# Kernel tuning notes

Hardware: AMD Instinct MI355X
Metric: run time of the kernel (lower is better)

## Reference

```python
import jax, jax.numpy as jnp
import numpy as np

B, S, D, H, F = 4, 2048, 1024, 16, 4096
HD = D // H
EPS = 1e-5


def _xavier(key, shape, fan_in, fan_out):
    a = float(np.sqrt(6.0 / (fan_in + fan_out)))
    return jax.random.uniform(key, shape, jnp.float32, -a, a)


def setup_inputs() -> dict:
    key = jax.random.key(0)
    ks = jax.random.split(key, 8)
    x = jax.random.normal(ks[0], (B, S, D), jnp.float32)
    # torch xavier_uniform on (1,H,D,HD) uses fan_in=D, fan_out=HD
    Wq = _xavier(ks[1], (H, D, HD), D, HD)
    Wk = _xavier(ks[2], (H, D, HD), D, HD)
    Wv = _xavier(ks[3], (H, D, HD), D, HD)
    Wo = _xavier(ks[4], (D, D), D, D)
    w_in = _xavier(ks[5], (D, F), D, F)
    b_in = jnp.zeros((F,), jnp.float32)
    w_out = _xavier(ks[6], (F, D), F, D)
    b_out = jnp.zeros((D,), jnp.float32)
    g1 = jnp.ones((D,), jnp.float32)
    be1 = jnp.zeros((D,), jnp.float32)
    g2 = jnp.ones((D,), jnp.float32)
    be2 = jnp.zeros((D,), jnp.float32)
    return {"x": x, "Wq": Wq, "Wk": Wk, "Wv": Wv, "Wo": Wo,
            "g1": g1, "be1": be1, "w_in": w_in, "b_in": b_in,
            "w_out": w_out, "b_out": b_out, "g2": g2, "be2": be2}


def _layernorm(x, g, b):
    mu = jnp.mean(x, axis=-1, keepdims=True)
    var = jnp.mean(jnp.square(x - mu), axis=-1, keepdims=True)
    return (x - mu) * jax.lax.rsqrt(var + EPS) * g + b


def reference(x, Wq, Wk, Wv, Wo, g1, be1, w_in, b_in, w_out, b_out, g2, be2):
    b, s, d = x.shape
    h, _, hd = Wq.shape
    q = jnp.einsum('bsd,hde->bhse', x, Wq)
    k = jnp.einsum('bsd,hde->bhse', x, Wk)
    v = jnp.einsum('bsd,hde->bhse', x, Wv)
    scores = jnp.einsum('bhse,bhte->bhst', q, k) / jnp.sqrt(jnp.float32(hd))
    causal = jnp.triu(jnp.ones((s, s), bool), k=1)  # [S,S]
    scores = jnp.where(causal, -jnp.inf, scores)
    p = jax.nn.softmax(scores, axis=-1)
    attn = jnp.einsum('bhst,bhte->bhse', p, v)
    # torch .view on contiguous (B,H,S,hd) -> (B,S,H*hd): plain reshape (no transpose)
    attn = attn.reshape(b, s, h * hd)
    attn = attn @ Wo
    x = _layernorm(x + attn, g1, be1)
    ffn = jax.nn.relu(x @ w_in + b_in) @ w_out + b_out
    x = _layernorm(x + ffn, g2, be2)
    return x
```

## Files before the change

### kernel.cpp

```cpp
#include <hip/hip_runtime.h>
#include <hip/hip_bf16.h>

typedef __hip_bfloat16 bf16;

#define BB 4
#define SS 2048
#define DD 1024
#define HH 16
#define FF 4096
#define HD 64
#define LN_EPS 1e-5f
#define QSCALE 0.1803368801111204f

typedef __attribute__((ext_vector_type(8))) __bf16 bf16x8;
typedef __attribute__((ext_vector_type(8))) unsigned short u16x8;
typedef __attribute__((ext_vector_type(4))) float f32x4;

__device__ __forceinline__ float cvt(float v) { return v; }
__device__ __forceinline__ float cvt(bf16 v) { return __bfloat162float(v); }
__device__ __forceinline__ void stf(float* p, float v) { *p = v; }
__device__ __forceinline__ void stf(bf16* p, float v) { *p = __float2bfloat16(v); }

__device__ __forceinline__ unsigned short f2bf_rne(float x) {
    unsigned int u = __float_as_uint(x);
    unsigned int r = (u + 0x7fffu + ((u >> 16) & 1u)) >> 16;
    return (unsigned short)r;
}

__device__ __forceinline__ void async_cp16(const void* g, void* l) {
    __builtin_amdgcn_global_load_lds(
        (const __attribute__((address_space(1))) unsigned int*)g,
        (__attribute__((address_space(3))) unsigned int*)l, 16, 0, 0);
}

__device__ __forceinline__ u16x8 ld_f32_chunk(const float* p) {
    const float4* q = (const float4*)p;
    const float4 a = q[0], b = q[1];
    u16x8 r;
    r[0] = f2bf_rne(a.x); r[1] = f2bf_rne(a.y); r[2] = f2bf_rne(a.z); r[3] = f2bf_rne(a.w);
    r[4] = f2bf_rne(b.x); r[5] = f2bf_rne(b.y); r[6] = f2bf_rne(b.z); r[7] = f2bf_rne(b.w);
    return r;
}

template <typename TA, typename TC, int EPI>
__launch_bounds__(256)
__global__ void mfma_gemm(const TA* __restrict__ A, const bf16* __restrict__ Bt,
                          TC* __restrict__ C, const float* __restrict__ bias,
                          const bf16* __restrict__ resb,
                          bf16* __restrict__ C2, bf16* __restrict__ C3,
                          int M, int N, int K, float oscale) {
    constexpr bool AF = (sizeof(TA) == 4);
    __shared__ unsigned short As[128 * 64];
    __shared__ unsigned short Bs[128 * 64];

    const int tid = threadIdx.x;
    const int lane = tid & 63;
    const int w = tid >> 6;
    const int wm = w >> 1, wn = w & 1;

    const int nwg = gridDim.x * gridDim.y;
    const int id = blockIdx.y * gridDim.x + blockIdx.x;
    const int cpx = nwg >> 3;
    const int swz = (id & 7) * cpx + (id >> 3);
    const int bx = swz % gridDim.x, by = swz / gridDim.x;
    const int m0 = by * 128, n0 = bx * 128;

    int ff[4], fr[4], fc[4], fg[4];
#pragma unroll
    for (int i = 0; i < 4; ++i) {
        ff[i] = tid + i * 256;
        fr[i] = ff[i] >> 3;
        fc[i] = ff[i] & 7;
        fg[i] = fc[i] ^ (fr[i] & 7);
    }

    f32x4 acc[4][4];
#pragma unroll
    for (int i = 0; i < 4; ++i)
#pragma unroll
        for (int j = 0; j < 4; ++j) acc[i][j] = (f32x4){0.f, 0.f, 0.f, 0.f};

    u16x8 sa[4];
    if (AF) {
#pragma unroll
        for (int i = 0; i < 4; ++i)
            sa[i] = ld_f32_chunk((const float*)A + (size_t)(m0 + fr[i]) * K + fg[i] * 8);
    }

    for (int k0 = 0; k0 < K; k0 += 64) {
        if (k0 > 0) __syncthreads();
        if (AF) {
#pragma unroll
            for (int i = 0; i < 4; ++i)
                *(u16x8*)&As[ff[i] * 8] = sa[i];
        } else {
#pragma unroll
            for (int i = 0; i < 4; ++i)
                async_cp16((const unsigned short*)A + (size_t)(m0 + fr[i]) * K + k0 + fg[i] * 8,
                           &As[ff[i] * 8]);
        }
#pragma unroll
        for (int i = 0; i < 4; ++i)
            async_cp16((const unsigned short*)Bt + (size_t)(n0 + fr[i]) * K + k0 + fg[i] * 8,
                       &Bs[ff[i] * 8]);
        __syncthreads();

        if (AF && k0 + 64 < K) {
            const int kn = k0 + 64;
#pragma unroll
            for (int i = 0; i < 4; ++i)
                sa[i] = ld_f32_chunk((const float*)A + (size_t)(m0 + fr[i]) * K + kn + fg[i] * 8);
        }

#pragma unroll
        for (int ks = 0; ks < 2; ++ks) {
            bf16x8 af[4], bfr[4];
#pragma unroll
            for (int i = 0; i < 4; ++i) {
                const int row = wm * 64 + i * 16 + (lane & 15);
                const int col = wn * 64 + i * 16 + (lane & 15);
                const int g = ks * 4 + (lane >> 4);
                af[i]  = *(const bf16x8*)&As[row * 64 + (g ^ (row & 7)) * 8];
                bfr[i] = *(const bf16x8*)&Bs[col * 64 + (g ^ (col & 7)) * 8];
            }
#pragma unroll
            for (int i = 0; i < 4; ++i)
#pragma unroll
                for (int j = 0; j < 4; ++j)
                    acc[i][j] = __builtin_amdgcn_mfma_f32_16x16x32_bf16(
                        af[i], bfr[j], acc[i][j], 0, 0, 0);
        }
    }

#pragma unroll
    for (int i = 0; i < 4; ++i) {
        const int mrow0 = m0 + wm * 64 + i * 16 + (lane >> 4) * 4;
#pragma unroll
        for (int j = 0; j < 4; ++j) {
            const int n = n0 + wn * 64 + j * 16 + (lane & 15);
            if (EPI == 5) {
                const int reg = n >> 10;
                const int nn = n & 1023;
                if (reg == 0) {
#pragma unroll
                    for (int r = 0; r < 4; ++r)
                        stf((bf16*)C + (size_t)(mrow0 + r) * 1024 + nn, acc[i][j][r] * oscale);
                } else if (reg == 1) {
#pragma unroll
                    for (int r = 0; r < 4; ++r)
                        stf(C2 + (size_t)(mrow0 + r) * 1024 + nn, acc[i][j][r]);
                } else {
                    const int bb = mrow0 >> 11, s = mrow0 & 2047;
                    ushort4 pk;
                    pk.x = f2bf_rne(acc[i][j][0]);
                    pk.y = f2bf_rne(acc[i][j][1]);
                    pk.z = f2bf_rne(acc[i][j][2]);
                    pk.w = f2bf_rne(acc[i][j][3]);
                    *(ushort4*)((unsigned short*)C3 + ((size_t)bb * 1024 + nn) * SS + s) = pk;
                }
            } else {
#pragma unroll
                for (int r = 0; r < 4; ++r) {
                    const size_t idx = (size_t)(mrow0 + r) * N + n;
                    float v = acc[i][j][r];
                    if (EPI == 0) v *= oscale;
                    if (EPI == 2) { v += bias[n]; v = fmaxf(v, 0.0f); }
                    if (EPI == 6) v += bias[n] + cvt(resb[idx]);
                    if (EPI == 7) v += cvt(resb[idx]);
                    stf(&C[idx], v);
                }
            }
        }
    }
}

__launch_bounds__(256)
__global__ void prep_kernel(const float* __restrict__ x,
                            const float* __restrict__ Wq, const float* __restrict__ Wk,
                            const float* __restrict__ Wv, const float* __restrict__ Wo,
                            const float* __restrict__ w_in, const float* __restrict__ w_out,
                            bf16* __restrict__ xb, bf16* __restrict__ WqkvT,
                            bf16* __restrict__ WoT, bf16* __restrict__ w_inT,
                            bf16* __restrict__ w_outT) {
    const int id = blockIdx.x;
    if (id < 8192) {
        const int i = id * 256 + threadIdx.x;
        const float4 v = ((const float4*)x)[i];
        ushort4 p;
        p.x = f2bf_rne(v.x); p.y = f2bf_rne(v.y); p.z = f2bf_rne(v.z); p.w = f2bf_rne(v.w);
        ((ushort4*)xb)[i] = p;
        return;
    }
    __shared__ float t[32][33];
    const int rem = id - 8192;
    const float* in;
    bf16* out;
    int R, C, bx, by;
    size_t in_o = 0, out_o = 0;
    if (rem < 3072) {
        const int z = rem >> 6, r2 = rem & 63;
        const int wi = z >> 4, head = z & 15;
        in = (wi == 0) ? Wq : (wi == 1) ? Wk : Wv;
        in_o = (size_t)head * DD * HD;
        out = WqkvT;
        out_o = (size_t)wi * DD * DD + (size_t)head * HD * DD;
        R = DD; C = HD;
        bx = (r2 & 1) * 32; by = (r2 >> 1) * 32;
    } else if (rem < 3072 + 1024) {
        const int r2 = rem - 3072;
        in = Wo; out = WoT; R = DD; C = DD;
        bx = (r2 & 31) * 32; by = (r2 >> 5) * 32;
    } else if (rem < 3072 + 1024 + 4096) {
        const int r2 = rem - 3072 - 1024;
        in = w_in; out = w_inT; R = DD; C = FF;
        bx = (r2 & 127) * 32; by = (r2 >> 7) * 32;
    } else {
        const int r2 = rem - 3072 - 1024 - 4096;
        in = w_out; out = w_outT; R = FF; C = DD;
        bx = (r2 & 31) * 32; by = (r2 >> 5) * 32;
    }
    const int tx = threadIdx.x & 31, ty = threadIdx.x >> 5;
#pragma unroll
    for (int i = 0; i < 32; i += 8)
        t[ty + i][tx] = in[in_o + (size_t)(by + ty + i) * C + bx + tx];
    __syncthreads();
#pragma unroll
    for (int i = 0; i < 32; i += 8)
        out[out_o + (size_t)(bx + ty + i) * R + by + tx] = __float2bfloat16(t[tx][ty + i]);
}

__launch_bounds__(256, 4)
__global__ void attn_mfma(const bf16* __restrict__ Q, const bf16* __restrict__ K,
                          const bf16* __restrict__ VT, bf16* __restrict__ O) {
    __shared__ unsigned short Ks[64 * 64];
    __shared__ unsigned short Vs[64 * 64];
    __shared__ unsigned short Ps[64 * 72];

    const int tid = threadIdx.x;
    const int lane = tid & 63;
    const int w = tid >> 6;
    const int ln = lane & 15;
    const int qd = lane >> 4;
    const int bh = blockIdx.x;
    const int b = bh >> 4;
    const int h = bh & 15;
    const int qi = 31 - blockIdx.y;
    const int q0 = qi * 64;

    bf16x8 aq[2];
    {
        const unsigned short* qp =
            (const unsigned short*)Q + ((size_t)b * SS + q0 + w * 16 + ln) * DD + h * HD;
        aq[0] = *(const bf16x8*)(qp + qd * 8);
        aq[1] = *(const bf16x8*)(qp + 32 + qd * 8);
    }

    int sf[2], sr[2], sg[2];
#pragma unroll
    for (int i = 0; i < 2; ++i) {
        sf[i] = tid + i * 256;
        sr[i] = sf[i] >> 3;
        sg[i] = (sf[i] & 7) ^ (sr[i] & 7);
    }
    const unsigned short* kbase = (const unsigned short*)K + (size_t)b * SS * DD + h * HD;
    const unsigned short* vbase = (const unsigned short*)VT + (size_t)(b * DD + h * HD) * SS;

    f32x4 oacc[4];
#pragma unroll
    for (int e = 0; e < 4; ++e) oacc[e] = (f32x4){0.f, 0.f, 0.f, 0.f};
    float l_r[4] = {0.f, 0.f, 0.f, 0.f};

    for (int kt = 0; kt <= qi; ++kt) {
        const int t0 = kt * 64;
        __syncthreads();
#pragma unroll
        for (int i = 0; i < 2; ++i) {
            async_cp16(kbase + (size_t)(t0 + sr[i]) * DD + sg[i] * 8, &Ks[sf[i] * 8]);
            async_cp16(vbase + (size_t)sr[i] * SS + t0 + sg[i] * 8, &Vs[sf[i] * 8]);
        }
        __syncthreads();

        f32x4 sfr[4];
#pragma unroll
        for (int ct = 0; ct < 4; ++ct) {
            const int row = ct * 16 + ln;
            const bf16x8 b0 = *(const bf16x8*)&Ks[row * 64 + ((qd) ^ (row & 7)) * 8];
            const bf16x8 b1 = *(const bf16x8*)&Ks[row * 64 + ((4 + qd) ^ (row & 7)) * 8];
            f32x4 t = __builtin_amdgcn_mfma_f32_16x16x32_bf16(
                aq[0], b0, (f32x4){0.f, 0.f, 0.f, 0.f}, 0, 0, 0);
            sfr[ct] = __builtin_amdgcn_mfma_f32_16x16x32_bf16(aq[1], b1, t, 0, 0, 0);
        }

        if (kt == qi) {
#pragma unroll
            for (int ct = 0; ct < 4; ++ct) {
                const int tg = t0 + ct * 16 + ln;
#pragma unroll
                for (int r = 0; r < 4; ++r) {
                    const int qg = q0 + w * 16 + qd * 4 + r;
                    if (tg > qg) sfr[ct][r] = -1e30f;
                }
            }
        }

#pragma unroll
        for (int ct = 0; ct < 4; ++ct)
#pragma unroll
            for (int r = 0; r < 4; ++r)
                sfr[ct][r] = __builtin_amdgcn_exp2f(sfr[ct][r]);
#pragma unroll
        for (int r = 0; r < 4; ++r)
            l_r[r] += (sfr[0][r] + sfr[1][r]) + (sfr[2][r] + sfr[3][r]);

#pragma unroll
        for (int ct = 0; ct < 4; ++ct)
#pragma unroll
            for (int r = 0; r < 4; ++r)
                Ps[(w * 16 + qd * 4 + r) * 72 + ct * 16 + ln] = f2bf_rne(sfr[ct][r]);
        const bf16x8 ap0 = *(const bf16x8*)&Ps[(w * 16 + ln) * 72 + qd * 8];
        const bf16x8 ap1 = *(const bf16x8*)&Ps[(w * 16 + ln) * 72 + 32 + qd * 8];

#pragma unroll
        for (int et = 0; et < 4; ++et) {
            const int row = et * 16 + ln;
            const bf16x8 v0 = *(const bf16x8*)&Vs[row * 64 + ((qd) ^ (row & 7)) * 8];
            const bf16x8 v1 = *(const bf16x8*)&Vs[row * 64 + ((4 + qd) ^ (row & 7)) * 8];
            oacc[et] = __builtin_amdgcn_mfma_f32_16x16x32_bf16(ap0, v0, oacc[et], 0, 0, 0);
            oacc[et] = __builtin_amdgcn_mfma_f32_16x16x32_bf16(ap1, v1, oacc[et], 0, 0, 0);
        }
    }

#pragma unroll
    for (int st = 1; st <= 8; st <<= 1)
#pragma unroll
        for (int r = 0; r < 4; ++r)
            l_r[r] += __shfl_xor(l_r[r], st);
    float linv[4];
#pragma unroll
    for (int r = 0; r < 4; ++r) linv[r] = 1.0f / l_r[r];
    unsigned short* ob = (unsigned short*)O + (size_t)bh * SS * HD;
#pragma unroll
    for (int et = 0; et < 4; ++et)
#pragma unroll
        for (int r = 0; r < 4; ++r) {
            const int qg = q0 + w * 16 + qd * 4 + r;
            ob[(size_t)qg * HD + et * 16 + ln] = f2bf_rne(oacc[et][r] * linv[r]);
        }
}

template <typename TIN, typename TOUT>
__launch_bounds__(256)
__global__ void ln_kernel(const TIN* __restrict__ X, TOUT* __restrict__ Y,
                          const float* __restrict__ g, const float* __restrict__ be) {
    const int row = blockIdx.x;
    const int tid = threadIdx.x;
    const int lane = tid & 63, w = tid >> 6;
    __shared__ float red[8];
    __shared__ float mv[2];

    float4 v;
    if (sizeof(TIN) == 4) {
        v = ((const float4*)((const float*)X + (size_t)row * DD))[tid];
    } else {
        const ushort4 u = ((const ushort4*)((const unsigned short*)X + (size_t)row * DD))[tid];
        v.x = __uint_as_float((unsigned)u.x << 16);
        v.y = __uint_as_float((unsigned)u.y << 16);
        v.z = __uint_as_float((unsigned)u.z << 16);
        v.w = __uint_as_float((unsigned)u.w << 16);
    }
    float s = (v.x + v.y) + (v.z + v.w);
    float q = (v.x * v.x + v.y * v.y) + (v.z * v.z + v.w * v.w);
#pragma unroll
    for (int st = 1; st < 64; st <<= 1) {
        s += __shfl_xor(s, st);
        q += __shfl_xor(q, st);
    }
    if (lane == 0) { red[w] = s; red[4 + w] = q; }
    __syncthreads();
    if (tid == 0) {
        const float ts = (red[0] + red[1]) + (red[2] + red[3]);
        const float tq = (red[4] + red[5]) + (red[6] + red[7]);
        const float mu = ts * (1.0f / DD);
        mv[0] = mu;
        mv[1] = rsqrtf(tq * (1.0f / DD) - mu * mu + LN_EPS);
    }
    __syncthreads();
    const float mu = mv[0], rs = mv[1];
    const float4 gg = ((const float4*)g)[tid];
    const float4 bb = ((const float4*)be)[tid];
    float o[4];
    o[0] = (v.x - mu) * rs * gg.x + bb.x;
    o[1] = (v.y - mu) * rs * gg.y + bb.y;
    o[2] = (v.z - mu) * rs * gg.z + bb.z;
    o[3] = (v.w - mu) * rs * gg.w + bb.w;
    if (sizeof(TOUT) == 4) {
        float4 of = {o[0], o[1], o[2], o[3]};
        ((float4*)((float*)Y + (size_t)row * DD))[tid] = of;
    } else {
        ushort4 p;
        p.x = f2bf_rne(o[0]); p.y = f2bf_rne(o[1]);
        p.z = f2bf_rne(o[2]); p.w = f2bf_rne(o[3]);
        ((ushort4*)((unsigned short*)Y + (size_t)row * DD))[tid] = p;
    }
}

extern "C" void kernel_launch(void* const* d_in, const int* in_sizes, int n_in,
                              void* d_out, int out_size, void* d_ws, size_t ws_size,
                              hipStream_t stream) {
    const float* x = (const float*)d_in[0];
    const float* Wq = (const float*)d_in[1];
    const float* Wk = (const float*)d_in[2];
    const float* Wv = (const float*)d_in[3];
    const float* Wo = (const float*)d_in[4];
    const float* g1 = (const float*)d_in[5];
    const float* be1 = (const float*)d_in[6];
    const float* w_in = (const float*)d_in[7];
    const float* b_in = (const float*)d_in[8];
    const float* w_out = (const float*)d_in[9];
    const float* b_out = (const float*)d_in[10];
    const float* g2 = (const float*)d_in[11];
    const float* be2 = (const float*)d_in[12];
    float* out = (float*)d_out;

    char* wsb = (char*)d_ws;
    const size_t MiB = 1u << 20;
    bf16* Qb = (bf16*)(wsb);
    bf16* Kb = (bf16*)(wsb + 16 * MiB);
    bf16* VT = (bf16*)(wsb + 32 * MiB);
    bf16* At = (bf16*)(wsb + 48 * MiB);
    bf16* xb = (bf16*)(wsb + 64 * MiB);
    bf16* X1b = (bf16*)(wsb + 80 * MiB);
    bf16* Hd = (bf16*)(wsb);
    bf16* X2b = (bf16*)(wsb + 64 * MiB);
    bf16* WqkvT = (bf16*)(wsb + 96 * MiB);
    bf16* WoT = (bf16*)(wsb + 102 * MiB);
    bf16* w_inT = (bf16*)(wsb + 104 * MiB);
    bf16* w_outT = (bf16*)(wsb + 112 * MiB);
    (void)ws_size;

    const int M = BB * SS;
    dim3 blk(256);

    prep_kernel<<<dim3(8192 + 3072 + 1024 + 4096 + 4096), blk, 0, stream>>>(
        x, Wq, Wk, Wv, Wo, w_in, w_out, xb, WqkvT, WoT, w_inT, w_outT);

    mfma_gemm<bf16, bf16, 5><<<dim3(3 * DD / 128, M / 128), blk, 0, stream>>>(
        xb, WqkvT, Qb, nullptr, nullptr, Kb, VT, M, 3 * DD, DD, QSCALE);

    attn_mfma<<<dim3(BB * HH, SS / 64), blk, 0, stream>>>(Qb, Kb, VT, At);

    mfma_gemm<bf16, bf16, 7><<<dim3(DD / 128, M / 128), blk, 0, stream>>>(
        At, WoT, X1b, nullptr, xb, nullptr, nullptr, M, DD, DD, 1.0f);
    ln_kernel<bf16, bf16><<<dim3(M), blk, 0, stream>>>(X1b, X1b, g1, be1);

    mfma_gemm<bf16, bf16, 2><<<dim3(FF / 128, M / 128), blk, 0, stream>>>(
        X1b, w_inT, Hd, b_in, nullptr, nullptr, nullptr, M, FF, DD, 1.0f);

    mfma_gemm<bf16, bf16, 6><<<dim3(DD / 128, M / 128), blk, 0, stream>>>(
        Hd, w_outT, X2b, b_out, X1b, nullptr, nullptr, M, DD, FF, 1.0f);

    ln_kernel<bf16, float><<<dim3(M), blk, 0, stream>>>(X2b, out, g2, be2);
}
```

Baseline: 462.4 us.

## Replace GEMM with 256-row double-buffered 8-wave kernel with async prefetch

Swaps the 128x128 single-buffered GEMM for a 256xBN tile kernel with 512 threads, double-buffered LDS, and direct global-to-LDS prefetch issued two k-tiles ahead, gated by explicit vmcnt waits and raw barriers. MFMA issue is split into four phases with raised wave priority, and the FFN up-projection uses a 256x256 tile. The aim is to hide global load latency behind MFMA work and raise arithmetic intensity per block. In exchange, LDS use and register pressure go up, and the larger tiles mean fewer workgroups for the smaller N=1024 GEMMs.

```diff
diff --git a/kernel.cpp b/kernel.cpp
--- a/kernel.cpp
+++ b/kernel.cpp
@@ -33,111 +33,146 @@
         (__attribute__((address_space(3))) unsigned int*)l, 16, 0, 0);
 }
 
-__device__ __forceinline__ u16x8 ld_f32_chunk(const float* p) {
-    const float4* q = (const float4*)p;
-    const float4 a = q[0], b = q[1];
-    u16x8 r;
-    r[0] = f2bf_rne(a.x); r[1] = f2bf_rne(a.y); r[2] = f2bf_rne(a.z); r[3] = f2bf_rne(a.w);
-    r[4] = f2bf_rne(b.x); r[5] = f2bf_rne(b.y); r[6] = f2bf_rne(b.z); r[7] = f2bf_rne(b.w);
-    return r;
-}
-
-template <typename TA, typename TC, int EPI>
-__launch_bounds__(256)
-__global__ void mfma_gemm(const TA* __restrict__ A, const bf16* __restrict__ Bt,
-                          TC* __restrict__ C, const float* __restrict__ bias,
-                          const bf16* __restrict__ resb,
-                          bf16* __restrict__ C2, bf16* __restrict__ C3,
-                          int M, int N, int K, float oscale) {
-    constexpr bool AF = (sizeof(TA) == 4);
-    __shared__ unsigned short As[128 * 64];
-    __shared__ unsigned short Bs[128 * 64];
+template <int N>
+__device__ __forceinline__ void s_wait_vmcnt() {
+    asm volatile("s_waitcnt vmcnt(%0)" ::"n"(N) : "memory");
+    __builtin_amdgcn_sched_barrier(0);
+}
+
+__device__ __forceinline__ void sync_raw() {
+    asm volatile("" ::: "memory");
+    __builtin_amdgcn_s_barrier();
+    asm volatile("" ::: "memory");
+    __builtin_amdgcn_sched_barrier(0);
+}
+
+template <int BN, int WM, int WN, int EPI>
+__launch_bounds__(512, 2)
+__global__ void gemm256(const bf16* __restrict__ Abf, const bf16* __restrict__ Bt,
+                        bf16* __restrict__ C, const float* __restrict__ bias,
+                        const bf16* __restrict__ resb,
+                        bf16* __restrict__ C2, bf16* __restrict__ C3,
+                        int M, int N, int K, float oscale) {
+    static_assert(WM * WN == 8, "8 waves");
+    constexpr int BM = 256;
+    constexpr int PWM = BM / WM;
+    constexpr int PWN = BN / WN;
+    constexpr int MI = PWM / 16;
+    constexpr int NJ = PWN / 16;
+    constexpr int ACH = BM * 8 / 512;
+    constexpr int BCH = BN * 8 / 512;
+    constexpr int LPT = ACH + BCH;
+
+    __shared__ unsigned short As[2][BM * 64];
+    __shared__ unsigned short Bs[2][BN * 64];
 
     const int tid = threadIdx.x;
     const int lane = tid & 63;
     const int w = tid >> 6;
-    const int wm = w >> 1, wn = w & 1;
+    const int wm = w / WN, wn = w % WN;
+    const int ln = lane & 15;
+    const int qd = lane >> 4;
 
     const int nwg = gridDim.x * gridDim.y;
     const int id = blockIdx.y * gridDim.x + blockIdx.x;
     const int cpx = nwg >> 3;
     const int swz = (id & 7) * cpx + (id >> 3);
     const int bx = swz % gridDim.x, by = swz / gridDim.x;
-    const int m0 = by * 128, n0 = bx * 128;
-
-    int ff[4], fr[4], fc[4], fg[4];
-#pragma unroll
-    for (int i = 0; i < 4; ++i) {
-        ff[i] = tid + i * 256;
-        fr[i] = ff[i] >> 3;
-        fc[i] = ff[i] & 7;
-        fg[i] = fc[i] ^ (fr[i] & 7);
-    }
-
-    f32x4 acc[4][4];
-#pragma unroll
-    for (int i = 0; i < 4; ++i)
-#pragma unroll
-        for (int j = 0; j < 4; ++j) acc[i][j] = (f32x4){0.f, 0.f, 0.f, 0.f};
-
-    u16x8 sa[4];
-    if (AF) {
-#pragma unroll
-        for (int i = 0; i < 4; ++i)
-            sa[i] = ld_f32_chunk((const float*)A + (size_t)(m0 + fr[i]) * K + fg[i] * 8);
-    }
-
-    for (int k0 = 0; k0 < K; k0 += 64) {
-        if (k0 > 0) __syncthreads();
-        if (AF) {
-#pragma unroll
-            for (int i = 0; i < 4; ++i)
-                *(u16x8*)&As[ff[i] * 8] = sa[i];
-        } else {
-#pragma unroll
-            for (int i = 0; i < 4; ++i)
-                async_cp16((const unsigned short*)A + (size_t)(m0 + fr[i]) * K + k0 + fg[i] * 8,
-                           &As[ff[i] * 8]);
-        }
-#pragma unroll
-        for (int i = 0; i < 4; ++i)
-            async_cp16((const unsigned short*)Bt + (size_t)(n0 + fr[i]) * K + k0 + fg[i] * 8,
-                       &Bs[ff[i] * 8]);
-        __syncthreads();
-
-        if (AF && k0 + 64 < K) {
-            const int kn = k0 + 64;
-#pragma unroll
-            for (int i = 0; i < 4; ++i)
-                sa[i] = ld_f32_chunk((const float*)A + (size_t)(m0 + fr[i]) * K + kn + fg[i] * 8);
-        }
-
-#pragma unroll
-        for (int ks = 0; ks < 2; ++ks) {
-            bf16x8 af[4], bfr[4];
-#pragma unroll
-            for (int i = 0; i < 4; ++i) {
-                const int row = wm * 64 + i * 16 + (lane & 15);
-                const int col = wn * 64 + i * 16 + (lane & 15);
-                const int g = ks * 4 + (lane >> 4);
-                af[i]  = *(const bf16x8*)&As[row * 64 + (g ^ (row & 7)) * 8];
-                bfr[i] = *(const bf16x8*)&Bs[col * 64 + (g ^ (col & 7)) * 8];
+    const int m0 = by * BM, n0 = bx * BN;
+
+    const unsigned short* Ag = (const unsigned short*)Abf;
+    const unsigned short* Bg = (const unsigned short*)Bt;
+
+    const unsigned short* agp[ACH];
+    const unsigned short* bgp[BCH];
+    int affo[ACH], bffo[BCH];
+#pragma unroll
+    for (int i = 0; i < ACH; ++i) {
+        const int ff = tid + i * 512, fr = ff >> 3, fg = (ff & 7) ^ (fr & 7);
+        agp[i] = Ag + (size_t)(m0 + fr) * K + fg * 8;
+        affo[i] = ff * 8;
+    }
+#pragma unroll
+    for (int i = 0; i < BCH; ++i) {
+        const int ff = tid + i * 512, fr = ff >> 3, fg = (ff & 7) ^ (fr & 7);
+        bgp[i] = Bg + (size_t)(n0 + fr) * K + fg * 8;
+        bffo[i] = ff * 8;
+    }
+
+    auto stage = [&](int kt, int buf) {
+        const int ko = kt * 64;
+#pragma unroll
+        for (int i = 0; i < ACH; ++i)
+            async_cp16(agp[i] + ko, &As[buf][affo[i]]);
+#pragma unroll
+        for (int i = 0; i < BCH; ++i)
+            async_cp16(bgp[i] + ko, &Bs[buf][bffo[i]]);
+    };
+
+    f32x4 acc[MI][NJ];
+#pragma unroll
+    for (int i = 0; i < MI; ++i)
+#pragma unroll
+        for (int j = 0; j < NJ; ++j) acc[i][j] = (f32x4){0.f, 0.f, 0.f, 0.f};
+
+    const int nt = K >> 6;
+    stage(0, 0);
+    stage(1, 1);
+
+    for (int t = 0; t < nt; ++t) {
+        if (t < nt - 1) s_wait_vmcnt<LPT>();
+        else            s_wait_vmcnt<0>();
+        sync_raw();
+
+        const int buf = t & 1;
+#pragma unroll
+        for (int ph = 0; ph < 4; ++ph) {
+            const int mh = ph >> 1, nh = ph & 1;
+            bf16x8 af[MI / 2][2], bq[NJ / 2][2];
+#pragma unroll
+            for (int i = 0; i < MI / 2; ++i) {
+                const int row = wm * PWM + (mh * (MI / 2) + i) * 16 + ln;
+#pragma unroll
+                for (int ks = 0; ks < 2; ++ks) {
+                    const int g = ks * 4 + qd;
+                    af[i][ks] = *(const bf16x8*)&As[buf][row * 64 + (g ^ (row & 7)) * 8];
+                }
             }
 #pragma unroll
-            for (int i = 0; i < 4; ++i)
-#pragma unroll
-                for (int j = 0; j < 4; ++j)
-                    acc[i][j] = __builtin_amdgcn_mfma_f32_16x16x32_bf16(
-                        af[i], bfr[j], acc[i][j], 0, 0, 0);
-        }
-    }
-
-#pragma unroll
-    for (int i = 0; i < 4; ++i) {
-        const int mrow0 = m0 + wm * 64 + i * 16 + (lane >> 4) * 4;
-#pragma unroll
-        for (int j = 0; j < 4; ++j) {
-            const int n = n0 + wn * 64 + j * 16 + (lane & 15);
+            for (int j = 0; j < NJ / 2; ++j) {
+                const int col = wn * PWN + (nh * (NJ / 2) + j) * 16 + ln;
+#pragma unroll
+                for (int ks = 0; ks < 2; ++ks) {
+                    const int g = ks * 4 + qd;
+                    bq[j][ks] = *(const bf16x8*)&Bs[buf][col * 64 + (g ^ (col & 7)) * 8];
+                }
+            }
+            __builtin_amdgcn_s_setprio(1);
+#pragma unroll
+            for (int ks = 0; ks < 2; ++ks)
+#pragma unroll
+                for (int i = 0; i < MI / 2; ++i)
+#pragma unroll
+                    for (int j = 0; j < NJ / 2; ++j)
+                        acc[mh * (MI / 2) + i][nh * (NJ / 2) + j] =
+                            __builtin_amdgcn_mfma_f32_16x16x32_bf16(
+                                af[i][ks], bq[j][ks],
+                                acc[mh * (MI / 2) + i][nh * (NJ / 2) + j], 0, 0, 0);
+            __builtin_amdgcn_s_setprio(0);
+            __builtin_amdgcn_sched_barrier(0);
+        }
+
+        asm volatile("s_waitcnt lgkmcnt(0)" ::: "memory");
+        sync_raw();
+        if (t + 2 < nt) stage(t + 2, buf);
+    }
+
+#pragma unroll
+    for (int i = 0; i < MI; ++i) {
+        const int mrow0 = m0 + wm * PWM + i * 16 + qd * 4;
+#pragma unroll
+        for (int j = 0; j < NJ; ++j) {
+            const int n = n0 + wn * PWN + j * 16 + ln;
             if (EPI == 5) {
                 const int reg = n >> 10;
                 const int nn = n & 1023;
@@ -163,7 +198,6 @@
                 for (int r = 0; r < 4; ++r) {
                     const size_t idx = (size_t)(mrow0 + r) * N + n;
                     float v = acc[i][j][r];
-                    if (EPI == 0) v *= oscale;
                     if (EPI == 2) { v += bias[n]; v = fmaxf(v, 0.0f); }
                     if (EPI == 6) v += bias[n] + cvt(resb[idx]);
                     if (EPI == 7) v += cvt(resb[idx]);
@@ -440,23 +474,24 @@
 
     const int M = BB * SS;
     dim3 blk(256);
+    dim3 blk512(512);
 
     prep_kernel<<<dim3(8192 + 3072 + 1024 + 4096 + 4096), blk, 0, stream>>>(
         x, Wq, Wk, Wv, Wo, w_in, w_out, xb, WqkvT, WoT, w_inT, w_outT);
 
-    mfma_gemm<bf16, bf16, 5><<<dim3(3 * DD / 128, M / 128), blk, 0, stream>>>(
+    gemm256<128, 4, 2, 5><<<dim3(3 * DD / 128, M / 256), blk512, 0, stream>>>(
         xb, WqkvT, Qb, nullptr, nullptr, Kb, VT, M, 3 * DD, DD, QSCALE);
 
     attn_mfma<<<dim3(BB * HH, SS / 64), blk, 0, stream>>>(Qb, Kb, VT, At);
 
-    mfma_gemm<bf16, bf16, 7><<<dim3(DD / 128, M / 128), blk, 0, stream>>>(
+    gemm256<128, 4, 2, 7><<<dim3(DD / 128, M / 256), blk512, 0, stream>>>(
         At, WoT, X1b, nullptr, xb, nullptr, nullptr, M, DD, DD, 1.0f);
     ln_kernel<bf16, bf16><<<dim3(M), blk, 0, stream>>>(X1b, X1b, g1, be1);
 
-    mfma_gemm<bf16, bf16, 2><<<dim3(FF / 128, M / 128), blk, 0, stream>>>(
+    gemm256<256, 2, 4, 2><<<dim3(FF / 256, M / 256), blk512, 0, stream>>>(
         X1b, w_inT, Hd, b_in, nullptr, nullptr, nullptr, M, FF, DD, 1.0f);
 
-    mfma_gemm<bf16, bf16, 6><<<dim3(DD / 128, M / 128), blk, 0, stream>>>(
+    gemm256<128, 4, 2, 6><<<dim3(DD / 128, M / 256), blk512, 0, stream>>>(
         Hd, w_outT, X2b, b_out, X1b, nullptr, nullptr, M, DD, FF, 1.0f);
 
     ln_kernel<bf16, float><<<dim3(M), blk, 0, stream>>>(X2b, out, g2, be2);
```

Result: slower. 493.8 us (+6.8%).

## Add double-buffered 8-wave 256-row GEMM kernel for QKV and FFN projections

Applied to the files above, without the earlier changes.

Adds a new GEMM kernel that uses 512 threads, 256-row tiles and double-buffered LDS. Loads for the next K tile are issued asynchronously and split into halves interleaved with two MFMA phases, using raw barriers, vmcnt waits and setprio. It replaces the 128x128 single-buffer GEMM for the QKV, FFN-in and FFN-out projections. The goal is to hide global-load latency and raise data reuse per tile, at the cost of more LDS and registers per block and fewer blocks in the grid.

```diff
diff --git a/kernel.cpp b/kernel.cpp
--- a/kernel.cpp
+++ b/kernel.cpp
@@ -33,6 +33,24 @@
         (__attribute__((address_space(3))) unsigned int*)l, 16, 0, 0);
 }
 
+template <int N>
+__device__ __forceinline__ void s_wait_vmcnt() {
+    asm volatile("s_waitcnt vmcnt(%0)" ::"n"(N) : "memory");
+    __builtin_amdgcn_sched_barrier(0);
+}
+
+__device__ __forceinline__ void sync_raw() {
+    asm volatile("" ::: "memory");
+    __builtin_amdgcn_s_barrier();
+    asm volatile("" ::: "memory");
+    __builtin_amdgcn_sched_barrier(0);
+}
+
+__device__ __forceinline__ void wait_lds() {
+    asm volatile("s_waitcnt lgkmcnt(0)" ::: "memory");
+    __builtin_amdgcn_sched_barrier(0);
+}
+
 __device__ __forceinline__ u16x8 ld_f32_chunk(const float* p) {
     const float4* q = (const float4*)p;
     const float4 a = q[0], b = q[1];
@@ -42,102 +60,159 @@
     return r;
 }
 
-template <typename TA, typename TC, int EPI>
-__launch_bounds__(256)
-__global__ void mfma_gemm(const TA* __restrict__ A, const bf16* __restrict__ Bt,
-                          TC* __restrict__ C, const float* __restrict__ bias,
-                          const bf16* __restrict__ resb,
-                          bf16* __restrict__ C2, bf16* __restrict__ C3,
-                          int M, int N, int K, float oscale) {
-    constexpr bool AF = (sizeof(TA) == 4);
-    __shared__ unsigned short As[128 * 64];
-    __shared__ unsigned short Bs[128 * 64];
+template <int BN, int WM, int WN, int EPI>
+__launch_bounds__(512, 2)
+__global__ void gemm8w(const bf16* __restrict__ Abf, const bf16* __restrict__ Bt,
+                       bf16* __restrict__ C, const float* __restrict__ bias,
+                       const bf16* __restrict__ resb,
+                       bf16* __restrict__ C2, bf16* __restrict__ C3,
+                       int M, int N, int K, float oscale) {
+    static_assert(WM * WN == 8, "8 waves");
+    constexpr int BM = 256;
+    constexpr int PWM = BM / WM;
+    constexpr int PWN = BN / WN;
+    constexpr int MI = PWM / 16;
+    constexpr int NJ = PWN / 16;
+    constexpr int MH = MI / 2;
+    constexpr int ALD = BM / 64;
+    constexpr int BLD = BN / 64;
+
+    __shared__ unsigned short As[2][BM * 64];
+    __shared__ unsigned short Bs[2][BN * 64];
 
     const int tid = threadIdx.x;
     const int lane = tid & 63;
     const int w = tid >> 6;
-    const int wm = w >> 1, wn = w & 1;
+    const int wm = w / WN, wn = w % WN;
+    const int ln = lane & 15;
+    const int qd = lane >> 4;
 
     const int nwg = gridDim.x * gridDim.y;
     const int id = blockIdx.y * gridDim.x + blockIdx.x;
     const int cpx = nwg >> 3;
     const int swz = (id & 7) * cpx + (id >> 3);
     const int bx = swz % gridDim.x, by = swz / gridDim.x;
-    const int m0 = by * 128, n0 = bx * 128;
-
-    int ff[4], fr[4], fc[4], fg[4];
-#pragma unroll
-    for (int i = 0; i < 4; ++i) {
-        ff[i] = tid + i * 256;
-        fr[i] = ff[i] >> 3;
-        fc[i] = ff[i] & 7;
-        fg[i] = fc[i] ^ (fr[i] & 7);
-    }
-
-    f32x4 acc[4][4];
-#pragma unroll
-    for (int i = 0; i < 4; ++i)
-#pragma unroll
-        for (int j = 0; j < 4; ++j) acc[i][j] = (f32x4){0.f, 0.f, 0.f, 0.f};
-
-    u16x8 sa[4];
-    if (AF) {
-#pragma unroll
-        for (int i = 0; i < 4; ++i)
-            sa[i] = ld_f32_chunk((const float*)A + (size_t)(m0 + fr[i]) * K + fg[i] * 8);
-    }
-
-    for (int k0 = 0; k0 < K; k0 += 64) {
-        if (k0 > 0) __syncthreads();
-        if (AF) {
-#pragma unroll
-            for (int i = 0; i < 4; ++i)
-                *(u16x8*)&As[ff[i] * 8] = sa[i];
+    const int m0 = by * BM, n0 = bx * BN;
+
+    const unsigned short* Ag = (const unsigned short*)Abf;
+    const unsigned short* Bg = (const unsigned short*)Bt;
+
+    const unsigned short* agp[ALD];
+    const unsigned short* bgp[BLD];
+    int aof[ALD], bof[BLD];
+#pragma unroll
+    for (int i = 0; i < ALD; ++i) {
+        const int ff = tid + i * 512, fr = ff >> 3, fg = (ff & 7) ^ (fr & 7);
+        agp[i] = Ag + (size_t)(m0 + fr) * K + fg * 8;
+        aof[i] = ff * 8;
+    }
+#pragma unroll
+    for (int i = 0; i < BLD; ++i) {
+        const int ff = tid + i * 512, fr = ff >> 3, fg = (ff & 7) ^ (fr & 7);
+        bgp[i] = Bg + (size_t)(n0 + fr) * K + fg * 8;
+        bof[i] = ff * 8;
+    }
+
+    auto stageA = [&](int kt, int buf) {
+#pragma unroll
+        for (int i = 0; i < ALD; ++i) async_cp16(agp[i] + kt * 64, &As[buf][aof[i]]);
+    };
+    auto stageBh = [&](int kt, int buf, int h) {
+#pragma unroll
+        for (int i = 0; i < BLD / 2; ++i) {
+            const int k = h * (BLD / 2) + i;
+            async_cp16(bgp[k] + kt * 64, &Bs[buf][bof[k]]);
+        }
+    };
+
+    f32x4 acc[MI][NJ];
+#pragma unroll
+    for (int i = 0; i < MI; ++i)
+#pragma unroll
+        for (int j = 0; j < NJ; ++j) acc[i][j] = (f32x4){0.f, 0.f, 0.f, 0.f};
+
+    const int nt = K >> 6;
+    stageA(0, 0);
+    stageBh(0, 0, 0);
+    stageBh(0, 0, 1);
+
+    for (int t = 0; t < nt; ++t) {
+        const int cur = t & 1, nxt = cur ^ 1;
+        if (t + 1 < nt) {
+            stageA(t + 1, nxt);
+            s_wait_vmcnt<ALD>();
         } else {
-#pragma unroll
-            for (int i = 0; i < 4; ++i)
-                async_cp16((const unsigned short*)A + (size_t)(m0 + fr[i]) * K + k0 + fg[i] * 8,
-                           &As[ff[i] * 8]);
-        }
-#pragma unroll
-        for (int i = 0; i < 4; ++i)
-            async_cp16((const unsigned short*)Bt + (size_t)(n0 + fr[i]) * K + k0 + fg[i] * 8,
-                       &Bs[ff[i] * 8]);
-        __syncthreads();
-
-        if (AF && k0 + 64 < K) {
-            const int kn = k0 + 64;
-#pragma unroll
-            for (int i = 0; i < 4; ++i)
-                sa[i] = ld_f32_chunk((const float*)A + (size_t)(m0 + fr[i]) * K + kn + fg[i] * 8);
-        }
-
-#pragma unroll
-        for (int ks = 0; ks < 2; ++ks) {
-            bf16x8 af[4], bfr[4];
-#pragma unroll
-            for (int i = 0; i < 4; ++i) {
-                const int row = wm * 64 + i * 16 + (lane & 15);
-                const int col = wn * 64 + i * 16 + (lane & 15);
-                const int g = ks * 4 + (lane >> 4);
-                af[i]  = *(const bf16x8*)&As[row * 64 + (g ^ (row & 7)) * 8];
-                bfr[i] = *(const bf16x8*)&Bs[col * 64 + (g ^ (col & 7)) * 8];
+            s_wait_vmcnt<0>();
+        }
+        sync_raw();
+
+        if (t + 1 < nt) stageBh(t + 1, nxt, 0);
+        bf16x8 bq[NJ][2];
+#pragma unroll
+        for (int j = 0; j < NJ; ++j) {
+            const int col = wn * PWN + j * 16 + ln;
+#pragma unroll
+            for (int ks = 0; ks < 2; ++ks) {
+                const int g = ks * 4 + qd;
+                bq[j][ks] = *(const bf16x8*)&Bs[cur][col * 64 + (g ^ (col & 7)) * 8];
             }
-#pragma unroll
-            for (int i = 0; i < 4; ++i)
-#pragma unroll
-                for (int j = 0; j < 4; ++j)
+        }
+        bf16x8 af0[MH][2];
+#pragma unroll
+        for (int i = 0; i < MH; ++i) {
+            const int row = wm * PWM + i * 16 + ln;
+#pragma unroll
+            for (int ks = 0; ks < 2; ++ks) {
+                const int g = ks * 4 + qd;
+                af0[i][ks] = *(const bf16x8*)&As[cur][row * 64 + (g ^ (row & 7)) * 8];
+            }
+        }
+        wait_lds();
+        __builtin_amdgcn_s_setprio(1);
+#pragma unroll
+        for (int ks = 0; ks < 2; ++ks)
+#pragma unroll
+            for (int i = 0; i < MH; ++i)
+#pragma unroll
+                for (int j = 0; j < NJ; ++j)
                     acc[i][j] = __builtin_amdgcn_mfma_f32_16x16x32_bf16(
-                        af[i], bfr[j], acc[i][j], 0, 0, 0);
-        }
-    }
-
-#pragma unroll
-    for (int i = 0; i < 4; ++i) {
-        const int mrow0 = m0 + wm * 64 + i * 16 + (lane >> 4) * 4;
-#pragma unroll
-        for (int j = 0; j < 4; ++j) {
-            const int n = n0 + wn * 64 + j * 16 + (lane & 15);
+                        af0[i][ks], bq[j][ks], acc[i][j], 0, 0, 0);
+        __builtin_amdgcn_s_setprio(0);
+        __builtin_amdgcn_sched_barrier(0);
+        sync_raw();
+
+        if (t + 1 < nt) stageBh(t + 1, nxt, 1);
+        bf16x8 af1[MH][2];
+#pragma unroll
+        for (int i = 0; i < MH; ++i) {
+            const int row = wm * PWM + (MH + i) * 16 + ln;
+#pragma unroll
+            for (int ks = 0; ks < 2; ++ks) {
+                const int g = ks * 4 + qd;
+                af1[i][ks] = *(const bf16x8*)&As[cur][row * 64 + (g ^ (row & 7)) * 8];
+            }
+        }
+        wait_lds();
+        __builtin_amdgcn_s_setprio(1);
+#pragma unroll
+        for (int ks = 0; ks < 2; ++ks)
+#pragma unroll
+            for (int i = 0; i < MH; ++i)
+#pragma unroll
+                for (int j = 0; j < NJ; ++j)
+                    acc[MH + i][j] = __builtin_amdgcn_mfma_f32_16x16x32_bf16(
+                        af1[i][ks], bq[j][ks], acc[MH + i][j], 0, 0, 0);
+        __builtin_amdgcn_s_setprio(0);
+        __builtin_amdgcn_sched_barrier(0);
+        sync_raw();
+    }
+
+#pragma unroll
+    for (int i = 0; i < MI; ++i) {
+        const int mrow0 = m0 + wm * PWM + i * 16 + qd * 4;
+#pragma unroll
+        for (int j = 0; j < NJ; ++j) {
+            const int n = n0 + wn * PWN + j * 16 + ln;
             if (EPI == 5) {
                 const int reg = n >> 10;
                 const int nn = n & 1023;
@@ -163,12 +238,120 @@
                 for (int r = 0; r < 4; ++r) {
                     const size_t idx = (size_t)(mrow0 + r) * N + n;
                     float v = acc[i][j][r];
-                    if (EPI == 0) v *= oscale;
                     if (EPI == 2) { v += bias[n]; v = fmaxf(v, 0.0f); }
                     if (EPI == 6) v += bias[n] + cvt(resb[idx]);
                     if (EPI == 7) v += cvt(resb[idx]);
                     stf(&C[idx], v);
                 }
+            }
+        }
+    }
+}
+
+template <typename TA, typename TC, int EPI>
+__launch_bounds__(256)
+__global__ void mfma_gemm(const TA* __restrict__ A, const bf16* __restrict__ Bt,
+                          TC* __restrict__ C, const float* __restrict__ bias,
+                          const bf16* __restrict__ resb,
+                          bf16* __restrict__ C2, bf16* __restrict__ C3,
+                          int M, int N, int K, float oscale) {
+    constexpr bool AF = (sizeof(TA) == 4);
+    __shared__ unsigned short As[128 * 64];
+    __shared__ unsigned short Bs[128 * 64];
+
+    const int tid = threadIdx.x;
+    const int lane = tid & 63;
+    const int w = tid >> 6;
+    const int wm = w >> 1, wn = w & 1;
+
+    const int nwg = gridDim.x * gridDim.y;
+    const int id = blockIdx.y * gridDim.x + blockIdx.x;
+    const int cpx = nwg >> 3;
+    const int swz = (id & 7) * cpx + (id >> 3);
+    const int bx = swz % gridDim.x, by = swz / gridDim.x;
+    const int m0 = by * 128, n0 = bx * 128;
+
+    int ff[4], fr[4], fg[4];
+#pragma unroll
+    for (int i = 0; i < 4; ++i) {
+        ff[i] = tid + i * 256;
+        fr[i] = ff[i] >> 3;
+        fg[i] = (ff[i] & 7) ^ (fr[i] & 7);
+    }
+
+    f32x4 acc[4][4];
+#pragma unroll
+    for (int i = 0; i < 4; ++i)
+#pragma unroll
+        for (int j = 0; j < 4; ++j) acc[i][j] = (f32x4){0.f, 0.f, 0.f, 0.f};
+
+    u16x8 sa[4];
+    if (AF) {
+#pragma unroll
+        for (int i = 0; i < 4; ++i)
+            sa[i] = ld_f32_chunk((const float*)A + (size_t)(m0 + fr[i]) * K + fg[i] * 8);
+    }
+
+    for (int k0 = 0; k0 < K; k0 += 64) {
+        if (k0 > 0) __syncthreads();
+        if (AF) {
+#pragma unroll
+            for (int i = 0; i < 4; ++i)
+                *(u16x8*)&As[ff[i] * 8] = sa[i];
+        } else {
+#pragma unroll
+            for (int i = 0; i < 4; ++i)
+                async_cp16((const unsigned short*)A + (size_t)(m0 + fr[i]) * K + k0 + fg[i] * 8,
+                           &As[ff[i] * 8]);
+        }
+#pragma unroll
+        for (int i = 0; i < 4; ++i)
+            async_cp16((const unsigned short*)Bt + (size_t)(n0 + fr[i]) * K + k0 + fg[i] * 8,
+                       &Bs[ff[i] * 8]);
+        __syncthreads();
+
+        if (AF && k0 + 64 < K) {
+            const int kn = k0 + 64;
+#pragma unroll
+            for (int i = 0; i < 4; ++i)
+                sa[i] = ld_f32_chunk((const float*)A + (size_t)(m0 + fr[i]) * K + kn + fg[i] * 8);
+        }
+
+#pragma unroll
+        for (int ks = 0; ks < 2; ++ks) {
+            bf16x8 af[4], bfr[4];
+#pragma unroll
+            for (int i = 0; i < 4; ++i) {
+                const int row = wm * 64 + i * 16 + (lane & 15);
+                const int col = wn * 64 + i * 16 + (lane & 15);
+                const int g = ks * 4 + (lane >> 4);
+                af[i]  = *(const bf16x8*)&As[row * 64 + (g ^ (row & 7)) * 8];
+                bfr[i] = *(const bf16x8*)&Bs[col * 64 + (g ^ (col & 7)) * 8];
+            }
+#pragma unroll
+            for (int i = 0; i < 4; ++i)
+#pragma unroll
+                for (int j = 0; j < 4; ++j)
+                    acc[i][j] = __builtin_amdgcn_mfma_f32_16x16x32_bf16(
+                        af[i], bfr[j], acc[i][j], 0, 0, 0);
+        }
+    }
+
+#pragma unroll
+    for (int i = 0; i < 4; ++i) {
+        const int mrow0 = m0 + wm * 64 + i * 16 + (lane >> 4) * 4;
+#pragma unroll
+        for (int j = 0; j < 4; ++j) {
+            const int n = n0 + wn * 64 + j * 16 + (lane & 15);
+#pragma unroll
+            for (int r = 0; r < 4; ++r) {
+                const size_t idx = (size_t)(mrow0 + r) * N + n;
+                float v = acc[i][j][r];
+                if (EPI == 0) v *= oscale;
+                if (EPI == 2) { v += bias[n]; v = fmaxf(v, 0.0f); }
+                if (EPI == 6) v += bias[n] + cvt(resb[idx]);
+                if (EPI == 7) v += cvt(resb[idx]);
+                stf(&C[idx], v);
             }
         }
     }
@@ -440,11 +623,12 @@
 
     const int M = BB * SS;
     dim3 blk(256);
+    dim3 blk512(512);
 
     prep_kernel<<<dim3(8192 + 3072 + 1024 + 4096 + 4096), blk, 0, stream>>>(
         x, Wq, Wk, Wv, Wo, w_in, w_out, xb, WqkvT, WoT, w_inT, w_outT);
 
-    mfma_gemm<bf16, bf16, 5><<<dim3(3 * DD / 128, M / 128), blk, 0, stream>>>(
+    gemm8w<256, 2, 4, 5><<<dim3(3 * DD / 256, M / 256), blk512, 0, stream>>>(
         xb, WqkvT, Qb, nullptr, nullptr, Kb, VT, M, 3 * DD, DD, QSCALE);
 
     attn_mfma<<<dim3(BB * HH, SS / 64), blk, 0, stream>>>(Qb, Kb, VT, At);
@@ -453,10 +637,10 @@
         At, WoT, X1b, nullptr, xb, nullptr, nullptr, M, DD, DD, 1.0f);
     ln_kernel<bf16, bf16><<<dim3(M), blk, 0, stream>>>(X1b, X1b, g1, be1);
 
-    mfma_gemm<bf16, bf16, 2><<<dim3(FF / 128, M / 128), blk, 0, stream>>>(
+    gemm8w<256, 2, 4, 2><<<dim3(FF / 256, M / 256), blk512, 0, stream>>>(
         X1b, w_inT, Hd, b_in, nullptr, nullptr, nullptr, M, FF, DD, 1.0f);
 
-    mfma_gemm<bf16, bf16, 6><<<dim3(DD / 128, M / 128), blk, 0, stream>>>(
+    gemm8w<128, 4, 2, 6><<<dim3(DD / 128, M / 256), blk512, 0, stream>>>(
         Hd, w_outT, X2b, b_out, X1b, nullptr, nullptr, M, DD, FF, 1.0f);
 
     ln_kernel<bf16, float><<<dim3(M), blk, 0, stream>>>(X2b, out, g2, be2);
```

New measurement: 534.6 us. 1.16x slower.
